# Performance work log

Hardware: AMD Instinct MI355X
Metric: run time of the kernel (lower is better)

Reference implementation:

```python
import jax, jax.numpy as jnp
import numpy as np

N = 20000      # num nodes
E = 320000     # num edges (avg degree 16)
R = 8          # num relations
D = 256        # input_dim / hidden dim
L = 6          # num_layers
EE = 32        # edge_embed_dim
B = 64         # batch size
K = 32         # num_negative + 1


def _layer_norm(x, g, b, eps=1e-5):
    mu = jnp.mean(x, axis=-1, keepdims=True)
    var = jnp.var(x, axis=-1, keepdims=True)
    return (x - mu) * jax.lax.rsqrt(var + eps) * g + b


def setup_inputs() -> dict:
    key = jax.random.key(0)
    ks = jax.random.split(key, 10)
    edge_index = jax.random.randint(ks[0], (2, E), 0, N)
    edge_type = jax.random.randint(ks[1], (E,), 0, R)
    edge_embed = jax.random.normal(ks[2], (E, EE), dtype=jnp.float32)
    src = jax.random.randint(ks[3], (B, K), 0, N)
    tgt = jax.random.randint(ks[4], (B, K), 0, N)
    rel = jax.random.randint(ks[5], (B, K), 0, R)
    batch = jnp.stack([src, tgt, rel], axis=-1)  # [B, K, 3]
    s = 1.0 / np.sqrt(D)
    W = jax.random.normal(ks[6], (L, R, D, D), dtype=jnp.float32) * s      # per-relation weights
    Wself = jax.random.normal(ks[7], (L, D, D), dtype=jnp.float32) * s     # self-loop weights
    We = jax.random.normal(ks[8], (L, EE, D), dtype=jnp.float32) * (1.0 / np.sqrt(EE))  # edge-embed proj (stage add)
    gamma = jnp.ones((L, D), dtype=jnp.float32)
    beta = jnp.zeros((L, D), dtype=jnp.float32)
    rel_emb = jax.random.normal(ks[9], (R, D), dtype=jnp.float32) * s      # DistMult relation embedding
    return dict(edge_index=edge_index, edge_type=edge_type, edge_embed=edge_embed,
                batch=batch, W=W, Wself=Wself, We=We, gamma=gamma, beta=beta,
                rel_emb=rel_emb)


def reference(edge_index, edge_type, edge_embed, batch, W, Wself, We, gamma, beta, rel_emb):
    src, dst = edge_index[0], edge_index[1]
    # mean aggregation denominator: in-degree per node (over all relations)
    deg = jnp.clip(jax.ops.segment_sum(jnp.ones((E,), jnp.float32), dst, num_segments=N), 1.0)
    # segment id combining relation and destination node -> aggregate-then-transform trick
    seg = edge_type * N + dst
    x = jnp.ones((N, D), dtype=jnp.float32)
    for l in range(L):
        # stage 'add': message = x[src] + proj(edge_embed)
        msg = x[src] + edge_embed @ We[l]                                  # [E, D]
        agg = jax.ops.segment_sum(msg, seg, num_segments=R * N).reshape(R, N, D)
        h = jnp.einsum('rnd,rdf->nf', agg, W[l]) / deg[:, None] + x @ Wself[l]
        h = jax.nn.relu(_layer_norm(h, gamma[l], beta[l]))
        x = h + x  # short_cut residual
    # DistMult scoring: gather source/target/relation embeddings, mul, sum
    s_emb = x[batch[..., 0]]          # [B, K, D]
    t_emb = x[batch[..., 1]]          # [B, K, D]
    r_emb = rel_emb[batch[..., 2]]    # [B, K, D]
    return jnp.sum(s_emb * r_emb * t_emb, axis=-1)  # [B, K]
```

## Files before the change

kernel.cpp:

```cpp
#include <hip/hip_runtime.h>
#include <hip/hip_bf16.h>

#define NN 20000
#define NP 20080
#define NE 320000
#define RR 8
#define DD 256
#define LL 6
#define EED 32
#define BB 64
#define KK 32
#define MM (NN * RR)
#define NSB 79
#define BMR 80
#define NGB 251
#define YROW 2304
#define YROWB 4608
#define HSTR 260
#define HSTRB 264

typedef __bf16 bf8 __attribute__((ext_vector_type(8)));
typedef float f4 __attribute__((ext_vector_type(4)));

__device__ inline float lo2f(unsigned v) { return __uint_as_float(v << 16); }
__device__ inline float hi2f(unsigned v) { return __uint_as_float(v & 0xffff0000u); }
__device__ inline unsigned short f2bf(float f) {
    unsigned u = __float_as_uint(f);
    return (unsigned short)((u + 0x7fff + ((u >> 16) & 1)) >> 16);
}
__device__ inline unsigned pack2(float lo, float hi) {
    return (unsigned)f2bf(lo) | ((unsigned)f2bf(hi) << 16);
}

#define GLOAD_LDS16(src, dst)                                                  \
    __builtin_amdgcn_global_load_lds(                                          \
        (const __attribute__((address_space(1))) unsigned int*)(src),          \
        (__attribute__((address_space(3))) unsigned int*)(dst), 16, 0, 0)

#define LGKM_BARRIER()                                                         \
    do {                                                                       \
        __builtin_amdgcn_sched_barrier(0);                                     \
        asm volatile("s_waitcnt lgkmcnt(0)");                                  \
        __builtin_amdgcn_s_barrier();                                          \
        __builtin_amdgcn_sched_barrier(0);                                     \
    } while (0)


__global__ __launch_bounds__(256) void hist_kernel(const int* __restrict__ dstv,
                                                   const int* __restrict__ typev,
                                                   int* __restrict__ hist) {
    int e = blockIdx.x * 256 + threadIdx.x;
    if (e < NE) atomicAdd(&hist[dstv[e] * 8 + typev[e]], 1);
}

__global__ __launch_bounds__(256) void scan1_kernel(const int* __restrict__ hist,
                                                    int* __restrict__ excl,
                                                    int* __restrict__ bsums) {
    __shared__ int tmp[256];
    int tid = threadIdx.x;
    int base = blockIdx.x * 2048 + tid * 8;
    int v[8]; int s = 0;
#pragma unroll
    for (int i = 0; i < 8; ++i) {
        v[i] = (base + i < MM) ? hist[base + i] : 0;
        s += v[i];
    }
    tmp[tid] = s;
    __syncthreads();
    for (int off = 1; off < 256; off <<= 1) {
        int t = (tid >= off) ? tmp[tid - off] : 0;
        __syncthreads();
        tmp[tid] += t;
        __syncthreads();
    }
    int run = tmp[tid] - s;
#pragma unroll
    for (int i = 0; i < 8; ++i) {
        if (base + i < MM) excl[base + i] = run;
        run += v[i];
    }
    if (tid == 255) bsums[blockIdx.x] = tmp[255];
}

__global__ __launch_bounds__(128) void scan2_kernel(int* __restrict__ bsums) {
    __shared__ int tmp[128];
    int tid = threadIdx.x;
    int orig = (tid < NSB) ? bsums[tid] : 0;
    tmp[tid] = orig;
    __syncthreads();
    for (int off = 1; off < 128; off <<= 1) {
        int t = (tid >= off) ? tmp[tid - off] : 0;
        __syncthreads();
        tmp[tid] += t;
        __syncthreads();
    }
    if (tid < NSB) bsums[tid] = tmp[tid] - orig;
}

__global__ __launch_bounds__(256) void add_off_kernel(const int* __restrict__ excl,
                                                      const int* __restrict__ bsums,
                                                      int* __restrict__ seg_start,
                                                      int* __restrict__ cursor) {
    int i = blockIdx.x * 256 + threadIdx.x;
    if (i < MM) {
        int v = excl[i] + bsums[i >> 11];
        seg_start[i] = v;
        cursor[i] = v;
    }
    if (i == 0) seg_start[MM] = NE;
}

__global__ __launch_bounds__(256) void sort_scatter_kernel(
    const int* __restrict__ srcv, const int* __restrict__ dstv,
    const int* __restrict__ typev, int* __restrict__ cursor,
    int* __restrict__ esrcY, int* __restrict__ eid) {
    int e = blockIdx.x * 256 + threadIdx.x;
    if (e < NE) {
        int key = dstv[e] * 8 + typev[e];
        int pos = atomicAdd(&cursor[key], 1);
        esrcY[pos] = srcv[e] * YROWB + typev[e] * 512;
        eid[pos]   = e;
    }
}

__global__ __launch_bounds__(256) void invdeg_kernel(const int* __restrict__ seg_start,
                                                     float* __restrict__ invdeg) {
    int i = blockIdx.x * 256 + threadIdx.x;
    if (i < NN) {
        int d = seg_start[i * 8 + 8] - seg_start[i * 8];
        invdeg[i] = 1.0f / (float)max(d, 1);
    }
}


__global__ __launch_bounds__(256) void eagg_kernel(
    const int* __restrict__ seg_start, const int* __restrict__ eid,
    const float* __restrict__ ee, const float* __restrict__ invdeg,
    unsigned short* __restrict__ eaggbf) {
    int tid = threadIdx.x;
    int s = blockIdx.x * 8 + (tid >> 5);
    int j = tid & 31;
    int n = s >> 3, r = s & 7;
    int j0 = seg_start[s], j1 = seg_start[s + 1];
    float sum = 0.0f;
#pragma unroll 1
    for (int p = j0; p < j1; p += 4) {
        int rem = j1 - p;
        int e4[4];
        float fv[4];
#pragma unroll
        for (int t = 0; t < 4; ++t)
            e4[t] = eid[(t < rem) ? p + t : p];
#pragma unroll
        for (int t = 0; t < 4; ++t)
            fv[t] = ee[(size_t)e4[t] * EED + j];
#pragma unroll
        for (int t = 0; t < 4; ++t)
            sum += (t < rem) ? fv[t] : 0.0f;
    }
    eaggbf[(size_t)n * DD + r * EED + j] = f2bf(sum * invdeg[n]);
}

__global__ __launch_bounds__(256) void whe_kernel(const float* __restrict__ We,
                                                  const float* __restrict__ W,
                                                  float* __restrict__ Whe) {
    __shared__ float WeS[EED * 32];
    int b = blockIdx.x;
    int l = b >> 6;
    int r = (b >> 3) & 7;
    int dc = b & 7;
    int tid = threadIdx.x;
    {
        int j = tid >> 3, dl = (tid & 7) * 4;
        *(float4*)&WeS[j * 32 + dl] =
            *(const float4*)&We[(size_t)l * EED * DD + (size_t)j * DD + dc * 32 + dl];
    }
    __syncthreads();
    const float* Wr = W + ((size_t)l * 8 + r) * DD * DD + (size_t)dc * 32 * DD;
    float acc[EED];
#pragma unroll
    for (int j = 0; j < EED; ++j) acc[j] = 0.0f;
    for (int dl = 0; dl < 32; ++dl) {
        float w = Wr[(size_t)dl * DD + tid];
#pragma unroll
        for (int j = 0; j < EED; ++j) acc[j] += WeS[j * 32 + dl] * w;
    }
    float* outp = Whe + (size_t)l * DD * DD + r * EED * DD + tid;
#pragma unroll
    for (int j = 0; j < EED; ++j) unsafeAtomicAdd(&outp[j * DD], acc[j]);
}

__global__ __launch_bounds__(256) void bswz_kernel(const float* __restrict__ W,
                                                   const float* __restrict__ Wself,
                                                   const float* __restrict__ Whe,
                                                   unsigned short* __restrict__ Bsw) {
    int gid = blockIdx.x * 256 + threadIdx.x;
    int f = gid & 255;
    int t = gid >> 8;
    int quad = t & 3; t >>= 2;
    int kb = t & 7; t >>= 3;
    int p = t % 10, l = t / 10;
    const float* base = (p <= 7) ? W + ((size_t)l * 8 + p) * DD * DD
                      : (p == 8) ? Wself + (size_t)l * DD * DD
                                 : Whe + (size_t)l * DD * DD;
    int k0 = kb * 32 + quad * 8;
    unsigned pk[4];
#pragma unroll
    for (int jj = 0; jj < 4; ++jj)
        pk[jj] = pack2(base[(size_t)(k0 + 2 * jj) * DD + f],
                       base[(size_t)(k0 + 2 * jj + 1) * DD + f]);
    uint4 v = make_uint4(pk[0], pk[1], pk[2], pk[3]);
    *(uint4*)&Bsw[(size_t)gid * 8] = v;
}

__global__ __launch_bounds__(256) void init_x_kernel(float* __restrict__ xA,
                                                     float* __restrict__ xB,
                                                     unsigned short* __restrict__ xbfA,
                                                     unsigned short* __restrict__ xbfB) {
    int i = blockIdx.x * 256 + threadIdx.x;
    ((float4*)xA)[i] = make_float4(1.f, 1.f, 1.f, 1.f);
    ((float4*)xB)[i] = make_float4(1.f, 1.f, 1.f, 1.f);
    ((uint2*)xbfA)[i] = make_uint2(0x3f803f80u, 0x3f803f80u);
    ((uint2*)xbfB)[i] = make_uint2(0x3f803f80u, 0x3f803f80u);
}

__global__ __launch_bounds__(512) void eterm6_kernel(
    const unsigned short* __restrict__ eaggbf, const unsigned short* __restrict__ Bsw,
    unsigned short* __restrict__ etermb6) {
    __shared__ __align__(16) unsigned char smem[40960 + BMR * HSTR * 4];
    unsigned char* As = smem;
    float* Hs = (float*)(smem + 40960);
    int tid = threadIdx.x;
    int wv = tid >> 6, lane = tid & 63;
    int row0 = blockIdx.x * BMR;
    int m = lane & 15, quad = lane >> 4;
    int col = wv * 32 + m;

#pragma unroll
    for (int i = 0; i < 5; ++i) {
        int bc = i * 512 + wv * 64;
        int c = bc + lane;
        int row = c >> 5, sc = c & 31, scs = sc ^ (row & 31);
        GLOAD_LDS16(eaggbf + (size_t)(row0 + row) * DD + scs * 8, As + (size_t)c * 16);
    }
    __syncthreads();

#pragma unroll 1
    for (int l = 0; l < LL; ++l) {
        const unsigned short* Bswl = Bsw + (size_t)l * 2560 * DD;
        bf8 breg[2][2];
#pragma unroll
        for (int nt = 0; nt < 2; ++nt) {
            breg[0][nt] = *(const bf8*)&Bswl[(((size_t)72 * 4 + quad) * 256 + col + nt * 16) * 8];
            breg[1][nt] = *(const bf8*)&Bswl[(((size_t)73 * 4 + quad) * 256 + col + nt * 16) * 8];
        }
        f4 acc[5][2] = {};
#pragma unroll
        for (int kb = 0; kb < 8; ++kb) {
            bf8 afr[5];
#pragma unroll
            for (int mt = 0; mt < 5; ++mt) {
                int rowl = mt * 16 + m;
                afr[mt] = *(bf8*)&As[rowl * 512 + (((kb * 4 + quad) ^ (rowl & 31)) * 16)];
            }
#pragma unroll
            for (int mt = 0; mt < 5; ++mt)
#pragma unroll
                for (int nt = 0; nt < 2; ++nt)
                    acc[mt][nt] = __builtin_amdgcn_mfma_f32_16x16x32_bf16(
                        afr[mt], breg[kb & 1][nt], acc[mt][nt], 0, 0, 0);
            int gn = 72 + kb + 2;
            if (gn < 80) {
#pragma unroll
                for (int nt = 0; nt < 2; ++nt)
                    breg[kb & 1][nt] = *(const bf8*)&Bswl[((size_t)gn * 4 + quad) * 2048
                                                          + ((size_t)(col + nt * 16)) * 8];
            }
        }
        if (l > 0) LGKM_BARRIER();
#pragma unroll
        for (int mt = 0; mt < 5; ++mt)
#pragma unroll
            for (int nt = 0; nt < 2; ++nt)
#pragma unroll
                for (int rg = 0; rg < 4; ++rg)
                    Hs[(mt * 16 + quad * 4 + rg) * HSTR + wv * 32 + nt * 16 + m] = acc[mt][nt][rg];
        LGKM_BARRIER();
        unsigned short* outl = etermb6 + (size_t)l * NP * DD;
#pragma unroll
        for (int c2 = 0; c2 < 10; ++c2) {
            int li = c2 * 512 + tid;
            int row = li >> 6, u4 = li & 63;
            float4 v = *(float4*)&Hs[row * HSTR + u4 * 4];
            *(uint2*)&outl[(size_t)(row0 + row) * DD + u4 * 4] =
                make_uint2(pack2(v.x, v.y), pack2(v.z, v.w));
        }
    }
}

__global__ __launch_bounds__(512) void ymm_kernel(
    const unsigned short* __restrict__ xbfin, const unsigned short* __restrict__ Bswl,
    unsigned short* __restrict__ Y) {
    __shared__ __align__(16) unsigned char smem[40960 + 40 * HSTRB * 2];
    unsigned char* As = smem;
    unsigned short* Hsb = (unsigned short*)(smem + 40960);
    int tid = threadIdx.x;
    int wv = tid >> 6, lane = tid & 63;
    int row0 = blockIdx.x * BMR;
    int m = lane & 15, quad = lane >> 4;

#pragma unroll
    for (int i = 0; i < 5; ++i) {
        int bc = i * 512 + wv * 64;
        int c = bc + lane;
        int row = c >> 5, sc = c & 31, scs = sc ^ (row & 31);
        GLOAD_LDS16(xbfin + (size_t)(row0 + row) * DD + scs * 8, As + (size_t)c * 16);
    }
    bf8 breg[2][2];
#pragma unroll
    for (int nt = 0; nt < 2; ++nt) {
        breg[0][nt] = *(const bf8*)&Bswl[((size_t)quad * 256 + wv * 32 + nt * 16 + m) * 8];
        breg[1][nt] = *(const bf8*)&Bswl[(((size_t)4 + quad) * 256 + wv * 32 + nt * 16 + m) * 8];
    }
    __syncthreads();

#pragma unroll 1
    for (int rt = 0; rt < 9; ++rt) {
        f4 acc[5][2] = {};
#pragma unroll
        for (int kb = 0; kb < 8; ++kb) {
            bf8 afr[5];
#pragma unroll
            for (int mt = 0; mt < 5; ++mt) {
                int rowl = mt * 16 + m;
                afr[mt] = *(bf8*)&As[rowl * 512 + (((kb * 4 + quad) ^ (rowl & 31)) * 16)];
            }
#pragma unroll
            for (int mt = 0; mt < 5; ++mt)
#pragma unroll
                for (int nt = 0; nt < 2; ++nt)
                    acc[mt][nt] = __builtin_amdgcn_mfma_f32_16x16x32_bf16(
                        afr[mt], breg[kb & 1][nt], acc[mt][nt], 0, 0, 0);
            int gn = rt * 8 + kb + 2;
            if (gn < 72) {
#pragma unroll
                for (int nt = 0; nt < 2; ++nt)
                    breg[kb & 1][nt] = *(const bf8*)&Bswl[((size_t)gn * 4 + quad) * 2048
                                                          + ((size_t)(wv * 32 + nt * 16 + m)) * 8];
            }
        }
#pragma unroll
        for (int p = 0; p < 2; ++p) {
            if (rt > 0 || p > 0) LGKM_BARRIER();
#pragma unroll
            for (int mt = 0; mt < 5; ++mt)
#pragma unroll
                for (int nt = 0; nt < 2; ++nt)
#pragma unroll
                    for (int rg = 0; rg < 4; ++rg) {
                        int r = mt * 16 + quad * 4 + rg;
                        if (r >= p * 40 && r < p * 40 + 40)
                            Hsb[(r - p * 40) * HSTRB + wv * 32 + nt * 16 + m] =
                                f2bf(acc[mt][nt][rg]);
                    }
            LGKM_BARRIER();
#pragma unroll
            for (int it = 0; it < 5; ++it) {
                int li = it * 512 + tid;
                int row = li >> 6, u4 = li & 63;
                uint2 v = *(uint2*)&Hsb[row * HSTRB + u4 * 4];
                *(uint2*)&Y[(size_t)(row0 + p * 40 + row) * YROW + rt * 256 + u4 * 4] = v;
            }
        }
    }
}

__global__ __launch_bounds__(512) void aggln_kernel(
    const int* __restrict__ seg_start, const int* __restrict__ esrcY,
    const unsigned short* __restrict__ Y, const unsigned short* __restrict__ eterml,
    const float* __restrict__ xin, const float* __restrict__ gl,
    const float* __restrict__ bl, float* __restrict__ xout,
    unsigned short* __restrict__ xbfout) {
    int tid = threadIdx.x;
    int wv = tid >> 6, lane = tid & 63;
    int n = blockIdx.x * 8 + wv;
    int j0 = seg_start[n * 8], j1 = seg_start[n * 8 + 8];
    float idg = 1.0f / (float)max(j1 - j0, 1);
    const char* Yb = (const char*)Y;
    size_t lo8 = (size_t)(lane * 8);
    size_t xi = (size_t)n * DD + lane * 4;
    uint2 sv = *(const uint2*)(Yb + (size_t)n * YROWB + 4096 + lo8);
    uint2 ev = *(const uint2*)&eterml[(size_t)n * DD + lane * 4];
    float4 xv = *(const float4*)&xin[xi];
    float4 g  = *(const float4*)&gl[lane * 4];
    float4 bb = *(const float4*)&bl[lane * 4];
    float a0 = 0.f, a1 = 0.f, a2 = 0.f, a3 = 0.f;
#pragma unroll 1
    for (int j = j0; j < j1; j += 16) {
        int rem = j1 - j;
        uint2 gvv[16];
#pragma unroll
        for (int t = 0; t < 16; ++t) {
            int jj = (t < rem) ? j + t : j;
            gvv[t] = *(const uint2*)(Yb + (size_t)(unsigned)esrcY[jj] + lo8);
        }
#pragma unroll
        for (int t = 0; t < 16; ++t) {
            unsigned vx = (t < rem) ? gvv[t].x : 0u;
            unsigned vy = (t < rem) ? gvv[t].y : 0u;
            a0 += lo2f(vx); a1 += hi2f(vx);
            a2 += lo2f(vy); a3 += hi2f(vy);
        }
    }
    float h0 = a0 * idg + lo2f(sv.x) + lo2f(ev.x);
    float h1 = a1 * idg + hi2f(sv.x) + hi2f(ev.x);
    float h2 = a2 * idg + lo2f(sv.y) + lo2f(ev.y);
    float h3 = a3 * idg + hi2f(sv.y) + hi2f(ev.y);
    float s = h0 + h1 + h2 + h3;
    float q = h0 * h0 + h1 * h1 + h2 * h2 + h3 * h3;
#pragma unroll
    for (int off = 32; off; off >>= 1) {
        s += __shfl_xor(s, off);
        q += __shfl_xor(q, off);
    }
    float mu  = s * (1.0f / DD);
    float var = q * (1.0f / DD) - mu * mu;
    float rs  = rsqrtf(var + 1e-5f);
    float4 o;
    o.x = fmaxf((h0 - mu) * rs * g.x + bb.x, 0.0f) + xv.x;
    o.y = fmaxf((h1 - mu) * rs * g.y + bb.y, 0.0f) + xv.y;
    o.z = fmaxf((h2 - mu) * rs * g.z + bb.z, 0.0f) + xv.z;
    o.w = fmaxf((h3 - mu) * rs * g.w + bb.w, 0.0f) + xv.w;
    *(float4*)&xout[xi] = o;
    *(uint2*)&xbfout[xi] = make_uint2(pack2(o.x, o.y), pack2(o.z, o.w));
}

__global__ __launch_bounds__(256) void score_kernel(
    const int* __restrict__ batch, const float* __restrict__ x,
    const float* __restrict__ rel_emb, float* __restrict__ out) {
    int tid = threadIdx.x;
    int wave = tid >> 6, lane = tid & 63;
    int idx = blockIdx.x * 4 + wave;
    int s = batch[idx * 3 + 0], t = batch[idx * 3 + 1], r = batch[idx * 3 + 2];
    float4 sv = *(const float4*)&x[(size_t)s * DD + lane * 4];
    float4 tv = *(const float4*)&x[(size_t)t * DD + lane * 4];
    float4 rv = *(const float4*)&rel_emb[(size_t)r * DD + lane * 4];
    float sum = sv.x * rv.x * tv.x + sv.y * rv.y * tv.y +
                sv.z * rv.z * tv.z + sv.w * rv.w * tv.w;
#pragma unroll
    for (int off = 32; off; off >>= 1) sum += __shfl_xor(sum, off);
    if (lane == 0) out[idx] = sum;
}

extern "C" void kernel_launch(void* const* d_in, const int* in_sizes, int n_in,
                              void* d_out, int out_size, void* d_ws, size_t ws_size,
                              hipStream_t stream) {
    const int*   edge_index = (const int*)d_in[0];
    const int*   srcv   = edge_index;
    const int*   dstv   = edge_index + NE;
    const int*   typev  = (const int*)d_in[1];
    const float* ee     = (const float*)d_in[2];
    const int*   batch  = (const int*)d_in[3];
    const float* W      = (const float*)d_in[4];
    const float* Wself  = (const float*)d_in[5];
    const float* We     = (const float*)d_in[6];
    const float* gamma  = (const float*)d_in[7];
    const float* beta   = (const float*)d_in[8];
    const float* rel_emb= (const float*)d_in[9];
    float* out = (float*)d_out;

    float* xA     = (float*)d_ws;
    float* xB     = xA + (size_t)NP * DD;
    float* Whe    = xB + (size_t)NP * DD;
    float* invdeg = Whe + (size_t)LL * DD * DD;
    unsigned short* xbfA   = (unsigned short*)(invdeg + NN);
    unsigned short* xbfB   = xbfA + (size_t)NP * DD;
    unsigned short* eaggbf = xbfB + (size_t)NP * DD;
    unsigned short* Bsw    = eaggbf + (size_t)NP * DD;
    int* hist      = (int*)(Bsw + (size_t)LL * 2560 * DD);
    int* excl      = hist + MM;
    int* seg_start = excl + MM;
    int* cursor    = seg_start + MM + 1;
    int* bsums     = cursor + MM;
    int* esrcY     = bsums + 256;
    int* eid       = esrcY + NE;
    unsigned short* etermb6 =
        (unsigned short*)(((uintptr_t)(eid + NE) + 255) & ~(uintptr_t)255);
    unsigned short* Y = etermb6 + (size_t)LL * NP * DD;

    hipMemsetAsync(hist, 0, MM * sizeof(int), stream);
    hist_kernel<<<(NE + 255) / 256, 256, 0, stream>>>(dstv, typev, hist);
    scan1_kernel<<<NSB, 256, 0, stream>>>(hist, excl, bsums);
    scan2_kernel<<<1, 128, 0, stream>>>(bsums);
    add_off_kernel<<<(MM + 255) / 256, 256, 0, stream>>>(excl, bsums, seg_start, cursor);
    invdeg_kernel<<<(NN + 255) / 256, 256, 0, stream>>>(seg_start, invdeg);
    sort_scatter_kernel<<<(NE + 255) / 256, 256, 0, stream>>>(srcv, dstv, typev, cursor, esrcY, eid);

    eagg_kernel<<<MM / 8, 256, 0, stream>>>(seg_start, eid, ee, invdeg, eaggbf);
    hipMemsetAsync(Whe, 0, (size_t)LL * DD * DD * sizeof(float), stream);
    whe_kernel<<<LL * 64, 256, 0, stream>>>(We, W, Whe);
    bswz_kernel<<<LL * 10 * 8 * 4, 256, 0, stream>>>(W, Wself, Whe, Bsw);
    init_x_kernel<<<(NP * DD / 4) / 256, 256, 0, stream>>>(xA, xB, xbfA, xbfB);
    eterm6_kernel<<<NGB, 512, 0, stream>>>(eaggbf, Bsw, etermb6);

    float* xin = xA;  float* xout = xB;
    unsigned short* xbin = xbfA;  unsigned short* xbout = xbfB;
    for (int l = 0; l < LL; ++l) {
        ymm_kernel<<<NGB, 512, 0, stream>>>(xbin, Bsw + (size_t)l * 2560 * DD, Y);
        aggln_kernel<<<NN / 8, 512, 0, stream>>>(seg_start, esrcY, Y,
            etermb6 + (size_t)l * NP * DD,
            xin, gamma + (size_t)l * DD, beta + (size_t)l * DD, xout, xbout);
        float* t = xin; xin = xout; xout = t;
        unsigned short* tb = xbin; xbin = xbout; xbout = tb;
    }
    score_kernel<<<(BB * KK) / 4, 256, 0, stream>>>(batch, xin, rel_emb, out);
}
```

Measured before the change: 773.8 us.

## Split ymm GEMM column halves across two blocks per row tile

The ymm kernel now launches twice as many blocks, each computing only 128 of the 256 output columns for an 80-row tile. Per-wave work drops to one 16-column MFMA tile, so there are fewer accumulators and fewer B loads. The epilogue writes in five 16-row chunks with a smaller, re-padded LDS staging buffer. The point is better CU occupancy and more parallelism, since 251 blocks underfill the GPU. The cost is that each block loads the A tile twice as often as before and hits more barriers in the epilogue.

```diff
diff --git a/kernel.cpp b/kernel.cpp
--- a/kernel.cpp
+++ b/kernel.cpp
@@ -14,10 +14,11 @@
 #define NSB 79
 #define BMR 80
 #define NGB 251
+#define NGB2 502
 #define YROW 2304
 #define YROWB 4608
 #define HSTR 260
-#define HSTRB 264
+#define HSTRB 272
 
 typedef __bf16 bf8 __attribute__((ext_vector_type(8)));
 typedef float f4 __attribute__((ext_vector_type(4)));
@@ -301,13 +302,15 @@
 __global__ __launch_bounds__(512) void ymm_kernel(
     const unsigned short* __restrict__ xbfin, const unsigned short* __restrict__ Bswl,
     unsigned short* __restrict__ Y) {
-    __shared__ __align__(16) unsigned char smem[40960 + 40 * HSTRB * 2];
+    __shared__ __align__(16) unsigned char smem[40960 + 16 * HSTRB * 2];
     unsigned char* As = smem;
     unsigned short* Hsb = (unsigned short*)(smem + 40960);
     int tid = threadIdx.x;
     int wv = tid >> 6, lane = tid & 63;
-    int row0 = blockIdx.x * BMR;
+    int nh = blockIdx.x & 1;
+    int row0 = (blockIdx.x >> 1) * BMR;
     int m = lane & 15, quad = lane >> 4;
+    int colb = nh * 128 + wv * 16 + m;
 
 #pragma unroll
     for (int i = 0; i < 5; ++i) {
@@ -316,17 +319,14 @@
         int row = c >> 5, sc = c & 31, scs = sc ^ (row & 31);
         GLOAD_LDS16(xbfin + (size_t)(row0 + row) * DD + scs * 8, As + (size_t)c * 16);
     }
-    bf8 breg[2][2];
-#pragma unroll
-    for (int nt = 0; nt < 2; ++nt) {
-        breg[0][nt] = *(const bf8*)&Bswl[((size_t)quad * 256 + wv * 32 + nt * 16 + m) * 8];
-        breg[1][nt] = *(const bf8*)&Bswl[(((size_t)4 + quad) * 256 + wv * 32 + nt * 16 + m) * 8];
-    }
+    bf8 breg[2];
+    breg[0] = *(const bf8*)&Bswl[((size_t)quad * 256 + colb) * 8];
+    breg[1] = *(const bf8*)&Bswl[(((size_t)4 + quad) * 256 + colb) * 8];
     __syncthreads();
 
 #pragma unroll 1
     for (int rt = 0; rt < 9; ++rt) {
-        f4 acc[5][2] = {};
+        f4 acc[5] = {};
 #pragma unroll
         for (int kb = 0; kb < 8; ++kb) {
             bf8 afr[5];
@@ -337,40 +337,23 @@
             }
 #pragma unroll
             for (int mt = 0; mt < 5; ++mt)
-#pragma unroll
-                for (int nt = 0; nt < 2; ++nt)
-                    acc[mt][nt] = __builtin_amdgcn_mfma_f32_16x16x32_bf16(
-                        afr[mt], breg[kb & 1][nt], acc[mt][nt], 0, 0, 0);
+                acc[mt] = __builtin_amdgcn_mfma_f32_16x16x32_bf16(
+                    afr[mt], breg[kb & 1], acc[mt], 0, 0, 0);
             int gn = rt * 8 + kb + 2;
-            if (gn < 72) {
-#pragma unroll
-                for (int nt = 0; nt < 2; ++nt)
-                    breg[kb & 1][nt] = *(const bf8*)&Bswl[((size_t)gn * 4 + quad) * 2048
-                                                          + ((size_t)(wv * 32 + nt * 16 + m)) * 8];
-            }
-        }
-#pragma unroll
-        for (int p = 0; p < 2; ++p) {
+            if (gn < 72)
+                breg[kb & 1] = *(const bf8*)&Bswl[((size_t)gn * 4 + quad) * 2048
+                                                  + (size_t)colb * 8];
+        }
+#pragma unroll
+        for (int p = 0; p < 5; ++p) {
             if (rt > 0 || p > 0) LGKM_BARRIER();
 #pragma unroll
-            for (int mt = 0; mt < 5; ++mt)
-#pragma unroll
-                for (int nt = 0; nt < 2; ++nt)
-#pragma unroll
-                    for (int rg = 0; rg < 4; ++rg) {
-                        int r = mt * 16 + quad * 4 + rg;
-                        if (r >= p * 40 && r < p * 40 + 40)
-                            Hsb[(r - p * 40) * HSTRB + wv * 32 + nt * 16 + m] =
-                                f2bf(acc[mt][nt][rg]);
-                    }
+            for (int rg = 0; rg < 4; ++rg)
+                Hsb[(quad * 4 + rg) * HSTRB + wv * 16 + m] = f2bf(acc[p][rg]);
             LGKM_BARRIER();
-#pragma unroll
-            for (int it = 0; it < 5; ++it) {
-                int li = it * 512 + tid;
-                int row = li >> 6, u4 = li & 63;
-                uint2 v = *(uint2*)&Hsb[row * HSTRB + u4 * 4];
-                *(uint2*)&Y[(size_t)(row0 + p * 40 + row) * YROW + rt * 256 + u4 * 4] = v;
-            }
+            int row = tid >> 5, u = tid & 31;
+            uint2 v = *(uint2*)&Hsb[row * HSTRB + u * 4];
+            *(uint2*)&Y[(size_t)(row0 + p * 16 + row) * YROW + rt * 256 + nh * 128 + u * 4] = v;
         }
     }
 }
@@ -506,7 +489,7 @@
     float* xin = xA;  float* xout = xB;
     unsigned short* xbin = xbfA;  unsigned short* xbout = xbfB;
     for (int l = 0; l < LL; ++l) {
-        ymm_kernel<<<NGB, 512, 0, stream>>>(xbin, Bsw + (size_t)l * 2560 * DD, Y);
+        ymm_kernel<<<NGB2, 512, 0, stream>>>(xbin, Bsw + (size_t)l * 2560 * DD, Y);
         aggln_kernel<<<NN / 8, 512, 0, stream>>>(seg_start, esrcY, Y,
             etermb6 + (size_t)l * NP * DD,
             xin, gamma + (size_t)l * DD, beta + (size_t)l * DD, xout, xbout);
```

Result: faster. 727.2 us (-6.0%).
